# Performance work log

Measured on AMD Instinct MI355X. Metric: run time of the kernel, lower is better.

Reference implementation:

```python
import jax, jax.numpy as jnp
import numpy as np

N_OBJ = 256   # number of RoIs/objects
C = 151       # num_obj_classes (Visual Genome)
H = 512       # hidden_dim == output_dim
T = 3         # time_step


def setup_inputs() -> dict:
    key = jax.random.key(0)
    ks = jax.random.split(key, 12)
    s = jnp.float32(0.02)

    def lin(k, out_dim, in_dim):
        k1, k2 = jax.random.split(k)
        w = jax.random.normal(k1, (out_dim, in_dim), jnp.float32) * s
        b = jax.random.normal(k2, (out_dim,), jnp.float32) * s
        return w, b

    inp = {}
    inp['input_ggnn'] = jax.random.normal(ks[0], (N_OBJ, H), jnp.float32)
    inp['matrix'] = jax.random.uniform(ks[1], (C, C), jnp.float32)
    for i, name in enumerate(['eq3_w', 'eq3_u', 'eq4_w', 'eq4_u', 'eq5_w', 'eq5_u']):
        in_dim = 2 * H if name.endswith('_w') else H
        w, b = lin(ks[2 + i], H, in_dim)
        inp['w_' + name] = w
        inp['b_' + name] = b
    w, b = lin(ks[8], H, 2 * H)
    inp['w_out'], inp['b_out'] = w, b
    w, b = lin(ks[9], C, C * H)
    inp['w_cls'], inp['b_cls'] = w, b
    return inp


def _ggnn_obj(input_ggnn, matrix,
              w_eq3_w, b_eq3_w, w_eq3_u, b_eq3_u,
              w_eq4_w, b_eq4_w, w_eq4_u, b_eq4_u,
              w_eq5_w, b_eq5_w, w_eq5_u, b_eq5_u,
              w_out, b_out, w_cls, b_cls):
    n = input_ggnn.shape[0]
    # hidden[i, c] = input_ggnn[i] for every class slot c  -> [N, C, H]
    hidden0 = jnp.broadcast_to(input_ggnn[:, None, :], (n, C, H))

    def step(hidden, _):
        hidden_sum = hidden.sum(axis=0)                # [C, H]
        x = hidden_sum[None, :, :] - hidden            # [N, C, H]
        # matrix.T @ x_i  and  matrix @ x_i, vectorized over N
        av1 = jnp.einsum('cd,nch->ndh', matrix, x)     # M^T propagation
        av2 = jnp.einsum('dc,nch->ndh', matrix, x)     # M propagation
        av = jnp.concatenate([av1, av2], axis=-1).reshape(n * C, 2 * H)
        h = hidden.reshape(n * C, H)
        zv = jax.nn.sigmoid(av @ w_eq3_w.T + b_eq3_w + h @ w_eq3_u.T + b_eq3_u)
        rv = jax.nn.sigmoid(av @ w_eq4_w.T + b_eq4_w + h @ w_eq4_u.T + b_eq4_u)
        hv = jnp.tanh(av @ w_eq5_w.T + b_eq5_w + (rv * h) @ w_eq5_u.T + b_eq5_u)
        h = (1.0 - zv) * h + zv * hv
        return h.reshape(n, C, H), None

    hidden, _ = jax.lax.scan(step, hidden0, None, length=T)

    inp_rep = hidden0.reshape(n * C, H)                # input repeated per class slot
    out = jnp.concatenate([hidden.reshape(n * C, H), inp_rep], axis=1)  # [N*C, 2H]
    out = jax.nn.relu(out @ w_out.T + b_out)           # [N*C, H]
    obj_dists = out.reshape(n, C * H) @ w_cls.T + b_cls  # [N, C]
    return obj_dists


def reference(input_ggnn, matrix,
              w_eq3_w, b_eq3_w, w_eq3_u, b_eq3_u,
              w_eq4_w, b_eq4_w, w_eq4_u, b_eq4_u,
              w_eq5_w, b_eq5_w, w_eq5_u, b_eq5_u,
              w_out, b_out, w_cls, b_cls):
    return _ggnn_obj(input_ggnn, matrix,
                     w_eq3_w, b_eq3_w, w_eq3_u, b_eq3_u,
                     w_eq4_w, b_eq4_w, w_eq4_u, b_eq4_u,
                     w_eq5_w, b_eq5_w, w_eq5_u, b_eq5_u,
                     w_out, b_out, w_cls, b_cls)
```

## Files before the change

### kernel.cpp

```cpp
#include <hip/hip_runtime.h>


#define C_     151
#define H_     512
#define NOBJ   256
#define NR     38656
#define NCH    64
#define CH     9664
#define CHP    9728
#define KPAD   160
#define KLDS   168
#define KA     2560
#define KV     3584
#define KB     2560

typedef _Float16 half8 __attribute__((ext_vector_type(8)));
typedef _Float16 half4 __attribute__((ext_vector_type(4)));
typedef float    f32x4 __attribute__((ext_vector_type(4)));

__device__ __forceinline__ float sigm(float x) { return 1.f / (1.f + expf(-x)); }

__device__ __forceinline__ void gload16(const void* g, void* l) {
    __builtin_amdgcn_global_load_lds(
        (const __attribute__((address_space(1))) void*)g,
        (__attribute__((address_space(3))) void*)l, 16, 0, 0);
}

__device__ __forceinline__ int kqswz(int s) {
    return 8 * (((s & 3) + 8 - ((s >> 2) & 3) - ((s >> 4) & 3)) & 3);
}
__device__ __forceinline__ int fraswz(int lane) {
    const int lb = lane & 15;
    return lb * 32 + 8 * (((lane >> 4) + lb + (lb >> 2)) & 3);
}

__device__ __forceinline__ half8 loadA8(const _Float16* p) { return *(const half8*)p; }
__device__ __forceinline__ half8 loadA8(const float* p) {
    f32x4 a = *(const f32x4*)p;
    f32x4 b = *(const f32x4*)(p + 4);
    half8 o;
    #pragma unroll
    for (int j = 0; j < 4; ++j) { o[j] = (_Float16)a[j]; o[4 + j] = (_Float16)b[j]; }
    return o;
}

template<int OP, typename AT, bool DUPK>
__global__ __launch_bounds__(256, 2)
void gemm_kernel(const AT* __restrict__ A, int lda,
                 const _Float16* __restrict__ B, int ldb,
                 void* __restrict__ Out, int ldo,
                 const float* __restrict__ bias,
                 const float* __restrict__ bias2,
                 int kchunk, int chunkStride)
{
    constexpr bool A16 = (sizeof(AT) == 2);
    __shared__ _Float16 sA[128 * 32];
    __shared__ _Float16 sB[128 * 32];
    const int tid  = threadIdx.x;
    const int lane = tid & 63;
    const int w    = tid >> 6;
    const int m0   = blockIdx.x * 128;
    const int n0   = blockIdx.y * 128;
    const int kbase = blockIdx.z * kchunk;

    const int s0 = tid, s1 = tid + 256;
    const AT* Ap0 = A + (size_t)(m0 + (s0 >> 2)) * lda + kqswz(s0);
    const AT* Ap1 = A + (size_t)(m0 + (s1 >> 2)) * lda + kqswz(s1);
    const _Float16* Bp0 = B + (size_t)(n0 + (s0 >> 2)) * ldb + kbase + kqswz(s0);
    const _Float16* Bp1 = B + (size_t)(n0 + (s1 >> 2)) * ldb + kbase + kqswz(s1);
    const int la0 = 8 * s0;
    const int la1 = 8 * s1;
    _Float16* lA0 = &sA[w * 512];
    _Float16* lA1 = &sA[2048 + w * 512];
    _Float16* lB0 = &sB[w * 512];
    _Float16* lB1 = &sB[2048 + w * 512];

    f32x4 acc[4][4];
    #pragma unroll
    for (int i = 0; i < 4; ++i)
        #pragma unroll
        for (int j = 0; j < 4; ++j)
            #pragma unroll
            for (int r = 0; r < 4; ++r) acc[i][j][r] = 0.f;

    const int mrow = (w >> 1) * 64;
    const int ncol = (w & 1) * 64;
    const int fra  = fraswz(lane);

    for (int k0 = 0; k0 < kchunk; k0 += 32) {
        int kA;
        if (DUPK) kA = (k0 < 2048) ? k0 : ((k0 < 3072) ? k0 - 2048 : k0 - 1024);
        else      kA = kbase + k0;
        if constexpr (A16) {
            __syncthreads();
            gload16(Ap0 + kA, lA0);
            gload16(Ap1 + kA, lA1);
            gload16(Bp0 + k0, lB0);
            gload16(Bp1 + k0, lB1);
            __syncthreads();
        } else {
            half8 va0 = loadA8(Ap0 + kA);
            half8 va1 = loadA8(Ap1 + kA);
            half8 vb0 = *(const half8*)(Bp0 + k0);
            half8 vb1 = *(const half8*)(Bp1 + k0);
            __syncthreads();
            *(half8*)&sA[la0] = va0;
            *(half8*)&sA[la1] = va1;
            *(half8*)&sB[la0] = vb0;
            *(half8*)&sB[la1] = vb1;
            __syncthreads();
        }
        half8 af[4], bf[4];
        #pragma unroll
        for (int i = 0; i < 4; ++i)
            af[i] = *(const half8*)&sA[(mrow + i * 16) * 32 + fra];
        #pragma unroll
        for (int i = 0; i < 4; ++i)
            bf[i] = *(const half8*)&sB[(ncol + i * 16) * 32 + fra];
        #pragma unroll
        for (int mi = 0; mi < 4; ++mi)
            #pragma unroll
            for (int ni = 0; ni < 4; ++ni)
                acc[mi][ni] = __builtin_amdgcn_mfma_f32_16x16x32_f16(af[mi], bf[ni], acc[mi][ni], 0, 0, 0);
    }

    const size_t zoff = (size_t)blockIdx.z * (size_t)chunkStride;
    #pragma unroll
    for (int mi = 0; mi < 4; ++mi) {
        #pragma unroll
        for (int ni = 0; ni < 4; ++ni) {
            #pragma unroll
            for (int r = 0; r < 4; ++r) {
                const int row = m0 + mrow + mi * 16 + (lane >> 4) * 4 + r;
                const int col = n0 + ncol + ni * 16 + (lane & 15);
                float v = acc[mi][ni][r];
                const size_t o = zoff + (size_t)row * ldo + col;
                if (OP == 0) {
                    ((float*)Out)[o] = v;
                } else if (OP == 1) {
                    ((_Float16*)Out)[o] = (_Float16)v;
                } else {
                    const unsigned n = (unsigned)row / 151u;
                    v += bias[col] + bias2[n * 512u + col];
                    v = v > 0.f ? v : 0.f;
                    ((_Float16*)Out)[o] = (_Float16)v;
                }
            }
        }
    }
}

__global__ __launch_bounds__(512, 2)
void gemm256(const _Float16* __restrict__ A, const _Float16* __restrict__ B,
             _Float16* __restrict__ Out)
{
    constexpr int LDA = KA;
    constexpr int LDB = KB;
    constexpr int LDO = 1536;
    constexpr int NT  = KV / 64;
    __shared__ _Float16 lds[2][32768];

    const int tid  = threadIdx.x;
    const int lane = tid & 63;
    const int w    = tid >> 6;

    const int lin  = blockIdx.y * gridDim.x + blockIdx.x;
    const int xcd  = lin & 7;
    const int sub  = lin >> 3;
    const int wgid = (xcd < 4 ? xcd * 29 : 4 * 29 + (xcd - 4) * 28) + sub;
    const int m0   = (wgid / 6) * 256;
    const int n0   = (wgid % 6) * 256;

    const int tr  = tid >> 3;
    const int swz = ((tid & 7) ^ (tr & 7)) << 3;
    const _Float16* Ap = A + (size_t)(m0 + tr) * LDA + swz;
    const _Float16* Bp = B + (size_t)(n0 + tr) * LDB + swz;
    const int ldsbase = w << 9;

    auto stage = [&](int buf, int kAb, int kBb) {
        _Float16* L = &lds[buf][0];
        gload16(Ap + kAb,                        L + ldsbase);
        gload16(Ap + (size_t)128 * LDA + kAb,    L + 128 * 64 + ldsbase);
        gload16(Bp + kBb,                        L + 16384 + ldsbase);
        gload16(Bp + (size_t)64  * LDB + kBb,    L + 16384 +  64 * 64 + ldsbase);
        gload16(Bp + (size_t)128 * LDB + kBb,    L + 16384 + 128 * 64 + ldsbase);
        gload16(Bp + (size_t)192 * LDB + kBb,    L + 16384 + 192 * 64 + ldsbase);
        gload16(Ap + (size_t)64  * LDA + kAb,    L +  64 * 64 + ldsbase);
        gload16(Ap + (size_t)192 * LDA + kAb,    L + 192 * 64 + ldsbase);
    };

    const int lb = lane & 15;
    const int lq = lane >> 4;
    auto frag = [&](const _Float16* base, int row0, int ks) -> half8 {
        const int row = row0 + lb;
        const int kg  = ks * 4 + lq;
        return *(const half8*)&base[row * 64 + ((kg ^ (row & 7)) << 3)];
    };

    const int wm = (w >> 2) * 128;
    const int wn = (w & 3) * 64;

    f32x4 acc[8][4];
    #pragma unroll
    for (int i = 0; i < 8; ++i)
        #pragma unroll
        for (int j = 0; j < 4; ++j)
            #pragma unroll
            for (int r = 0; r < 4; ++r) acc[i][j][r] = 0.f;

    half8 aL[4][2], aH[4][2], bA[2][2], bB[2][2];

#define PHASE_MFMA(AF, BF, MO, NO) do {                                         \
    __builtin_amdgcn_s_setprio(1);                                              \
    _Pragma("unroll")                                                           \
    for (int i = 0; i < 4; ++i) {                                               \
        _Pragma("unroll")                                                       \
        for (int j = 0; j < 2; ++j) {                                           \
            _Pragma("unroll")                                                   \
            for (int ks = 0; ks < 2; ++ks)                                      \
                acc[(MO) + i][(NO) + j] =                                       \
                    __builtin_amdgcn_mfma_f32_16x16x32_f16(                     \
                        AF[i][ks], BF[j][ks], acc[(MO) + i][(NO) + j], 0, 0, 0);\
        }                                                                       \
    }                                                                           \
    __builtin_amdgcn_s_setprio(0);                                              \
} while (0)

    stage(0, 0, 0);

    for (int t = 0; t < NT; ++t) {
        const _Float16* sA = &lds[t & 1][0];
        const _Float16* sB = &lds[t & 1][16384];

        asm volatile("s_waitcnt vmcnt(2)" ::: "memory");
        __builtin_amdgcn_s_barrier();
        __builtin_amdgcn_sched_barrier(0);
        if (t + 1 < NT) {
            const int kk  = (t + 1) * 64;
            const int kAb = (kk < 2048) ? kk : ((kk < 3072) ? kk - 2048 : kk - 1024);
            const int kBb = (kk < 1024) ? kk : kk - 1024;
            stage((t + 1) & 1, kAb, kBb);
        }
        #pragma unroll
        for (int i = 0; i < 4; ++i) {
            aL[i][0] = frag(sA, wm + i * 16, 0);
            aL[i][1] = frag(sA, wm + i * 16, 1);
        }
        #pragma unroll
        for (int j = 0; j < 2; ++j) {
            bA[j][0] = frag(sB, wn + j * 16, 0);
            bA[j][1] = frag(sB, wn + j * 16, 1);
        }
        #pragma unroll
        for (int j = 0; j < 2; ++j) {
            bB[j][0] = frag(sB, wn + 32 + j * 16, 0);
            bB[j][1] = frag(sB, wn + 32 + j * 16, 1);
        }
        PHASE_MFMA(aL, bA, 0, 0);
        PHASE_MFMA(aL, bB, 0, 2);

        if (t + 1 < NT) asm volatile("s_waitcnt vmcnt(8)" ::: "memory");
        else            asm volatile("s_waitcnt vmcnt(0)" ::: "memory");
        __builtin_amdgcn_s_barrier();
        __builtin_amdgcn_sched_barrier(0);
        #pragma unroll
        for (int i = 0; i < 4; ++i) {
            aH[i][0] = frag(sA, wm + 64 + i * 16, 0);
            aH[i][1] = frag(sA, wm + 64 + i * 16, 1);
        }
        PHASE_MFMA(aH, bA, 4, 0);
        PHASE_MFMA(aH, bB, 4, 2);
    }
#undef PHASE_MFMA

    #pragma unroll
    for (int mi = 0; mi < 8; ++mi) {
        #pragma unroll
        for (int ni = 0; ni < 4; ++ni) {
            #pragma unroll
            for (int r = 0; r < 4; ++r) {
                const int row = m0 + wm + mi * 16 + (lane >> 4) * 4 + r;
                const int col = n0 + wn + ni * 16 + (lane & 15);
                Out[(size_t)row * LDO + col] = (_Float16)acc[mi][ni][r];
            }
        }
    }
}

__global__ __launch_bounds__(256, 2)
void mix_kernel(const float* __restrict__ hid, const float* __restrict__ S,
                const _Float16* __restrict__ MTh, const _Float16* __restrict__ MTl,
                const _Float16* __restrict__ Mrh, const _Float16* __restrict__ Mrl,
                _Float16* __restrict__ AVH, int cbase)
{
    __shared__ _Float16 sxh[64 * KLDS];
    __shared__ _Float16 sxl[64 * KLDS];
    const int n  = blockIdx.x;
    const int h0 = blockIdx.y * 64;
    const int tid = threadIdx.x;

    #pragma unroll
    for (int i = 0; i < 5; ++i) {
        const int s  = tid + 256 * i;
        const int c  = s >> 3;
        const int hg = s & 7;
        half8 oh, ol;
        if (c < C_) {
            const float* hp = &hid[(size_t)(cbase + n * C_ + c) * H_ + h0 + hg * 8];
            const float* sp = &S[c * H_ + h0 + hg * 8];
            half8 hh;
            #pragma unroll
            for (int j = 0; j < 8; ++j) {
                const float hv = hp[j];
                const float x = sp[j] - hv;
                const _Float16 hi = (_Float16)x;
                oh[j] = hi;
                ol[j] = (_Float16)(x - (float)hi);
                hh[j] = (_Float16)hv;
            }
            *(half8*)&AVH[(size_t)(n * C_ + c) * KA + 2048 + h0 + hg * 8] = hh;
        } else {
            #pragma unroll
            for (int j = 0; j < 8; ++j) { oh[j] = (_Float16)0.f; ol[j] = (_Float16)0.f; }
        }
        #pragma unroll
        for (int j = 0; j < 8; ++j) {
            sxh[(hg * 8 + j) * KLDS + c] = oh[j];
            sxl[(hg * 8 + j) * KLDS + c] = ol[j];
        }
    }
    __syncthreads();

    const int lane = tid & 63;
    const int w    = tid >> 6;
    const _Float16* Mhi = (w >> 1) ? Mrh : MTh;
    const _Float16* Mlo = (w >> 1) ? Mrl : MTl;
    const int hb = (w & 1) * 32;

    f32x4 acc[10][2];
    #pragma unroll
    for (int i = 0; i < 10; ++i)
        #pragma unroll
        for (int j = 0; j < 2; ++j)
            #pragma unroll
            for (int r = 0; r < 4; ++r) acc[i][j][r] = 0.f;

    #pragma unroll
    for (int pass = 0; pass < 3; ++pass) {
        const _Float16* Ma = (pass == 2) ? Mlo : Mhi;
        const _Float16* X  = (pass == 1) ? sxl : sxh;
        #pragma unroll
        for (int kk = 0; kk < 5; ++kk) {
            const int k0 = kk * 32;
            half8 bf[2];
            #pragma unroll
            for (int ht = 0; ht < 2; ++ht)
                bf[ht] = *(const half8*)&X[(hb + ht * 16 + (lane & 15)) * KLDS + k0 + 8 * (lane >> 4)];
            #pragma unroll
            for (int dt = 0; dt < 10; ++dt) {
                half8 af = *(const half8*)&Ma[(dt * 16 + (lane & 15)) * KPAD + k0 + 8 * (lane >> 4)];
                acc[dt][0] = __builtin_amdgcn_mfma_f32_16x16x32_f16(af, bf[0], acc[dt][0], 0, 0, 0);
                acc[dt][1] = __builtin_amdgcn_mfma_f32_16x16x32_f16(af, bf[1], acc[dt][1], 0, 0, 0);
            }
        }
    }

    const int mixoff = (w >> 1) * 512;
    #pragma unroll
    for (int dt = 0; dt < 10; ++dt) {
        #pragma unroll
        for (int ht = 0; ht < 2; ++ht) {
            #pragma unroll
            for (int r = 0; r < 4; ++r) {
                const int d = dt * 16 + (lane >> 4) * 4 + r;
                if (d < C_) {
                    const int h = h0 + hb + ht * 16 + (lane & 15);
                    const float v = acc[dt][ht][r];
                    const _Float16 hi = (_Float16)v;
                    const _Float16 lo = (_Float16)(v - (float)hi);
                    _Float16* rowp = AVH + (size_t)(n * C_ + d) * KA + mixoff + h;
                    rowp[0]    = hi;
                    rowp[1024] = lo;
                }
            }
        }
    }
}


__global__ void k_sreduce(const float* __restrict__ hid, float* __restrict__ Stmp)
{
    const int c  = blockIdx.x;
    const int g  = blockIdx.y;
    const int hw = threadIdx.x;
    const float* p = hid + (size_t)c * H_ + hw * 8;
    float s[8];
    #pragma unroll
    for (int j = 0; j < 8; ++j) s[j] = 0.f;
    const size_t stride = (size_t)C_ * H_;
    for (int n = g * 32; n < g * 32 + 32; ++n) {
        f32x4 a = *(const f32x4*)(p + (size_t)n * stride);
        f32x4 b = *(const f32x4*)(p + (size_t)n * stride + 4);
        #pragma unroll
        for (int j = 0; j < 4; ++j) { s[j] += a[j]; s[4 + j] += b[j]; }
    }
    float* o = Stmp + (size_t)g * (C_ * H_) + c * H_ + hw * 8;
    *(f32x4*)o       = f32x4{s[0], s[1], s[2], s[3]};
    *(f32x4*)(o + 4) = f32x4{s[4], s[5], s[6], s[7]};
}

__global__ void k_sfold(const float* __restrict__ Stmp, float* __restrict__ S)
{
    const int idx = blockIdx.x * 256 + threadIdx.x;
    float s = 0.f;
    #pragma unroll
    for (int g = 0; g < 8; ++g) s += Stmp[(size_t)g * (C_ * H_) + idx];
    S[idx] = s;
}

__global__ void k_ew1(_Float16* __restrict__ pre, const float* __restrict__ hid,
                      const float* __restrict__ bz, const float* __restrict__ br, int cbase)
{
    const int idx = blockIdx.x * 256 + threadIdx.x;
    const unsigned r = idx >> 7;
    const int o4 = (idx & 127) << 2;
    const size_t base = (size_t)r * 1536;
    half4 zp = *(const half4*)&pre[base + o4];
    half4 rp = *(const half4*)&pre[base + 512 + o4];
    f32x4 hd = *(const f32x4*)&hid[(size_t)(cbase + r) * H_ + o4];
    f32x4 bz4 = *(const f32x4*)&bz[o4];
    f32x4 br4 = *(const f32x4*)&br[o4];
    half4 zs, rh;
    #pragma unroll
    for (int j = 0; j < 4; ++j) {
        float z = sigm((float)zp[j] + bz4[j]);
        float rr = sigm((float)rp[j] + br4[j]);
        zs[j] = (_Float16)z;
        rh[j] = (_Float16)(rr * hd[j]);
    }
    *(half4*)&pre[base + o4] = zs;
    *(half4*)&pre[base + 512 + o4] = rh;
}

__global__ void k_ew2(const _Float16* __restrict__ pre, const _Float16* __restrict__ p5a,
                      const _Float16* __restrict__ p5b,
                      float* __restrict__ hid, const float* __restrict__ b5, int cbase)
{
    const int idx = blockIdx.x * 256 + threadIdx.x;
    const unsigned r = idx >> 7;
    const int o4 = (idx & 127) << 2;
    const size_t base = (size_t)r * 1536;
    half4 w5 = *(const half4*)&pre[base + 1024 + o4];
    half4 pa = *(const half4*)&p5a[(size_t)r * H_ + o4];
    half4 pb = *(const half4*)&p5b[(size_t)r * H_ + o4];
    half4 zz = *(const half4*)&pre[base + o4];
    f32x4 hd = *(const f32x4*)&hid[(size_t)(cbase + r) * H_ + o4];
    f32x4 b54 = *(const f32x4*)&b5[o4];
    #pragma unroll
    for (int j = 0; j < 4; ++j) {
        float t = tanhf((float)w5[j] + (float)pa[j] + (float)pb[j] + b54[j]);
        float z = (float)zz[j];
        hd[j] = (1.f - z) * hd[j] + z * t;
    }
    *(f32x4*)&hid[(size_t)(cbase + r) * H_ + o4] = hd;
}


__global__ void prep_wbig(const float* w3w, const float* w3u,
                          const float* w4w, const float* w4u,
                          const float* w5w, const float* w5u,
                          _Float16* __restrict__ Wbig)
{
    const int idx = blockIdx.x * 256 + threadIdx.x;
    const int op = idx / KB;
    const int j = idx - op * KB;
    const int g = op >> 9, o = op & 511;
    const float* ww = (g == 0) ? w3w : (g == 1) ? w4w : w5w;
    const float* wu = (g == 0) ? w3u : (g == 1) ? w4u : w5u;
    _Float16 out;
    if (j < 1024) {
        out = (_Float16)ww[o * 1024 + j];
    } else if (j < 2048) {
        const float v = ww[o * 1024 + (j - 1024)];
        const _Float16 hi = (_Float16)v;
        out = (_Float16)(v - (float)hi);
    } else {
        out = (g < 2) ? (_Float16)wu[o * 512 + (j - 2048)] : (_Float16)0.f;
    }
    Wbig[idx] = out;
}

__global__ void prep_m(const float* __restrict__ matrix,
                       _Float16* __restrict__ MTh, _Float16* __restrict__ MTl,
                       _Float16* __restrict__ Mrh, _Float16* __restrict__ Mrl)
{
    const int idx = blockIdx.x * 256 + threadIdx.x;
    const int d = idx / KPAD, c = idx - d * KPAD;
    float vT = 0.f, vR = 0.f;
    if (d < C_ && c < C_) { vT = matrix[c * C_ + d]; vR = matrix[d * C_ + c]; }
    const _Float16 th = (_Float16)vT;
    const _Float16 rh = (_Float16)vR;
    MTh[idx] = th; MTl[idx] = (_Float16)(vT - (float)th);
    Mrh[idx] = rh; Mrl[idx] = (_Float16)(vR - (float)rh);
}

__global__ void prep_wout(const float* __restrict__ wout,
                          _Float16* __restrict__ WL, _Float16* __restrict__ WR)
{
    const int idx = blockIdx.x * 256 + threadIdx.x;
    const int o = idx >> 9, j = idx & 511;
    WL[idx] = (_Float16)wout[o * 1024 + j];
    WR[idx] = (_Float16)wout[o * 1024 + 512 + j];
}

__global__ void prep_wcls(const float* __restrict__ wcls, _Float16* __restrict__ w16)
{
    const int k = blockIdx.x * 256 + threadIdx.x;
    const int d = blockIdx.y;
    w16[(size_t)d * (C_ * H_) + k] = (_Float16)wcls[(size_t)d * (C_ * H_) + k];
}

__global__ void k_cast(const float* __restrict__ src, _Float16* __restrict__ dst, int n)
{
    const int i = blockIdx.x * 256 + threadIdx.x;
    if (i < n) dst[i] = (_Float16)src[i];
}

__global__ void prep_bias(const float* b3w, const float* b3u, const float* b4w,
                          const float* b4u, const float* b5w, const float* b5u,
                          float* bz, float* br, float* b5)
{
    const int i = threadIdx.x;
    bz[i] = b3w[i] + b3u[i];
    br[i] = b4w[i] + b4u[i];
    b5[i] = b5w[i] + b5u[i];
}

__global__ void prep_hid(const float* __restrict__ input, float* __restrict__ hid)
{
    const int idx = blockIdx.x * 256 + threadIdx.x;
    const unsigned row = idx >> 7;
    const int h4 = (idx & 127) << 2;
    const unsigned n = row / 151u;
    f32x4 v = *(const f32x4*)&input[(size_t)n * H_ + h4];
    *(f32x4*)&hid[(size_t)row * H_ + h4] = v;
}

__global__ void k_reduce(const float* __restrict__ partial, const float* __restrict__ bcls,
                         float* __restrict__ out)
{
    const int idx = blockIdx.x * 256 + threadIdx.x;
    const unsigned n = (unsigned)idx / 151u;
    const unsigned d = (unsigned)idx - n * 151u;
    float s = 0.f;
    for (int z = 0; z < C_; ++z)
        s += partial[(size_t)z * (NOBJ * 256) + n * 256 + d];
    out[idx] = s + bcls[d];
}


extern "C" void kernel_launch(void* const* d_in, const int* in_sizes, int n_in,
                              void* d_out, int out_size, void* d_ws, size_t ws_size,
                              hipStream_t stream)
{
    const float* input  = (const float*)d_in[0];
    const float* matrix = (const float*)d_in[1];
    const float* w3w = (const float*)d_in[2];
    const float* b3w = (const float*)d_in[3];
    const float* w3u = (const float*)d_in[4];
    const float* b3u = (const float*)d_in[5];
    const float* w4w = (const float*)d_in[6];
    const float* b4w = (const float*)d_in[7];
    const float* w4u = (const float*)d_in[8];
    const float* b4u = (const float*)d_in[9];
    const float* w5w = (const float*)d_in[10];
    const float* b5w = (const float*)d_in[11];
    const float* w5u = (const float*)d_in[12];
    const float* b5u = (const float*)d_in[13];
    const float* wout = (const float*)d_in[14];
    const float* bout = (const float*)d_in[15];
    const float* wcls = (const float*)d_in[16];
    const float* bcls = (const float*)d_in[17];
    float* obj = (float*)d_out;

    char* ws = (char*)d_ws;
    size_t off = 0;
    auto take = [&](size_t bytes) -> char* {
        off = (off + 255) & ~(size_t)255;
        char* p = ws + off;
        off += bytes;
        return p;
    };

    _Float16* Wbig  = (_Float16*)take((size_t)1536 * KB * 2);
    _Float16* MTh   = (_Float16*)take((size_t)KPAD * KPAD * 2);
    _Float16* MTl   = (_Float16*)take((size_t)KPAD * KPAD * 2);
    _Float16* Mrh   = (_Float16*)take((size_t)KPAD * KPAD * 2);
    _Float16* Mrl   = (_Float16*)take((size_t)KPAD * KPAD * 2);
    _Float16* W5u16 = (_Float16*)take((size_t)512 * 512 * 2);
    _Float16* WL16  = (_Float16*)take((size_t)512 * 512 * 2);
    _Float16* WR16  = (_Float16*)take((size_t)512 * 512 * 2);
    _Float16* in16  = (_Float16*)take((size_t)256 * 512 * 2);
    float*    bz    = (float*)take(512 * 4);
    float*    br    = (float*)take(512 * 4);
    float*    b5    = (float*)take(512 * 4);
    float*    Stmp  = (float*)take((size_t)8 * C_ * H_ * 4);
    float*    S32   = (float*)take((size_t)C_ * H_ * 4);
    float*    base  = (float*)take((size_t)256 * 512 * 4);
    float*    hid32 = (float*)take((size_t)NR * H_ * 4);
    _Float16* AVH   = (_Float16*)take((size_t)CHP * KA * 2);
    _Float16* prec  = (_Float16*)take((size_t)CHP * 1536 * 2);
    _Float16* p5u = AVH;
    _Float16* OUT16 = AVH;
    _Float16* Wcls16 = (_Float16*)hid32;
    float* partial = (float*)((char*)hid32 + (size_t)NOBJ * C_ * H_ * 2);

    (void)in_sizes; (void)n_in; (void)out_size; (void)ws_size;

    prep_wbig<<<dim3((1536 * KB) / 256), 256, 0, stream>>>(w3w, w3u, w4w, w4u, w5w, w5u, Wbig);
    prep_m<<<dim3((KPAD * KPAD) / 256), 256, 0, stream>>>(matrix, MTh, MTl, Mrh, Mrl);
    k_cast<<<dim3((512 * 512) / 256), 256, 0, stream>>>(w5u, W5u16, 512 * 512);
    prep_wout<<<dim3((512 * 512) / 256), 256, 0, stream>>>(wout, WL16, WR16);
    k_cast<<<dim3((256 * 512) / 256), 256, 0, stream>>>(input, in16, 256 * 512);
    prep_bias<<<dim3(1), 512, 0, stream>>>(b3w, b3u, b4w, b4u, b5w, b5u, bz, br, b5);
    prep_hid<<<dim3((NR * 128) / 256), 256, 0, stream>>>(input, hid32);
    gemm_kernel<0, _Float16, false><<<dim3(2, 4, 1), 256, 0, stream>>>(
        in16, 512, WR16, 512, base, 512, nullptr, nullptr, 512, 0);

    for (int t = 0; t < 3; ++t) {
        k_sreduce<<<dim3(C_, 8), 64, 0, stream>>>(hid32, Stmp);
        k_sfold<<<dim3((C_ * H_) / 256), 256, 0, stream>>>(Stmp, S32);
        for (int cc = 0; cc < 4; ++cc) {
            const int cbase = cc * CH;
            mix_kernel<<<dim3(NCH, 8), 256, 0, stream>>>(
                hid32, S32, MTh, MTl, Mrh, Mrl, AVH, cbase);
            gemm256<<<dim3(CHP / 256, 1536 / 256, 1), 512, 0, stream>>>(
                AVH, Wbig, prec);
            k_ew1<<<dim3((CH * 128) / 256), 256, 0, stream>>>(prec, hid32, bz, br, cbase);
            gemm_kernel<1, _Float16, false><<<dim3(CHP / 128, 4, 2), 256, 0, stream>>>(
                prec + 512, 1536, W5u16, 512, p5u, 512, nullptr, nullptr, 256, CHP * 512);
            k_ew2<<<dim3((CH * 128) / 256), 256, 0, stream>>>(
                prec, p5u, p5u + (size_t)CHP * 512, hid32, b5, cbase);
        }
    }

    gemm_kernel<2, float, false><<<dim3(NR / 128, 512 / 128, 1), 256, 0, stream>>>(
        hid32, 512, WL16, 512, OUT16, 512, bout, base, 512, 0);

    prep_wcls<<<dim3((C_ * H_) / 256, C_), 256, 0, stream>>>(wcls, Wcls16);
    gemm_kernel<0, _Float16, false><<<dim3(NOBJ / 128, 256 / 128, C_), 256, 0, stream>>>(
        OUT16, C_ * H_, Wcls16, C_ * H_, partial, 256, nullptr, nullptr, 512, NOBJ * 256);
    k_reduce<<<dim3(NR / 256), 256, 0, stream>>>(partial, bcls, obj);
}
```

Before: 2.416 ms.

## Load GEMM B fragments directly into registers, keep only A in LDS

The gemm256 kernel now stages only the A tile through LDS. Each wave loads its B fragments straight from global memory into double-buffered registers, prefetching the next K-tile while computing the current one. This halves the LDS footprint, which may let two workgroups fit per CU. It also removes the mid-tile barrier and wait. In exchange it adds register pressure on top of the already large accumulator set, and waves sharing columns issue duplicate global B reads that rely on cache hits.

```diff
diff --git a/kernel.cpp b/kernel.cpp
--- a/kernel.cpp
+++ b/kernel.cpp
@@ -158,7 +158,7 @@
     constexpr int LDB = KB;
     constexpr int LDO = 1536;
     constexpr int NT  = KV / 64;
-    __shared__ _Float16 lds[2][32768];
+    __shared__ _Float16 lds[2][16384];
 
     const int tid  = threadIdx.x;
     const int lane = tid & 63;
@@ -174,19 +174,14 @@
     const int tr  = tid >> 3;
     const int swz = ((tid & 7) ^ (tr & 7)) << 3;
     const _Float16* Ap = A + (size_t)(m0 + tr) * LDA + swz;
-    const _Float16* Bp = B + (size_t)(n0 + tr) * LDB + swz;
     const int ldsbase = w << 9;
 
-    auto stage = [&](int buf, int kAb, int kBb) {
+    auto stageA = [&](int buf, int kAb) {
         _Float16* L = &lds[buf][0];
-        gload16(Ap + kAb,                        L + ldsbase);
-        gload16(Ap + (size_t)128 * LDA + kAb,    L + 128 * 64 + ldsbase);
-        gload16(Bp + kBb,                        L + 16384 + ldsbase);
-        gload16(Bp + (size_t)64  * LDB + kBb,    L + 16384 +  64 * 64 + ldsbase);
-        gload16(Bp + (size_t)128 * LDB + kBb,    L + 16384 + 128 * 64 + ldsbase);
-        gload16(Bp + (size_t)192 * LDB + kBb,    L + 16384 + 192 * 64 + ldsbase);
-        gload16(Ap + (size_t)64  * LDA + kAb,    L +  64 * 64 + ldsbase);
-        gload16(Ap + (size_t)192 * LDA + kAb,    L + 192 * 64 + ldsbase);
+        gload16(Ap + kAb,                     L + ldsbase);
+        gload16(Ap + (size_t)64  * LDA + kAb, L +  64 * 64 + ldsbase);
+        gload16(Ap + (size_t)128 * LDA + kAb, L + 128 * 64 + ldsbase);
+        gload16(Ap + (size_t)192 * LDA + kAb, L + 192 * 64 + ldsbase);
     };
 
     const int lb = lane & 15;
@@ -200,6 +195,8 @@
     const int wm = (w >> 2) * 128;
     const int wn = (w & 3) * 64;
 
+    const _Float16* Bb = B + (size_t)(n0 + wn + lb) * LDB + lq * 8;
+
     f32x4 acc[8][4];
     #pragma unroll
     for (int i = 0; i < 8; ++i)
@@ -208,7 +205,20 @@
             #pragma unroll
             for (int r = 0; r < 4; ++r) acc[i][j][r] = 0.f;
 
-    half8 aL[4][2], aH[4][2], bA[2][2], bB[2][2];
+    half8 a[4][2];
+    half8 b0A[2][2], b0B[2][2];
+    half8 b1A[2][2], b1B[2][2];
+
+#define LOADB(BA, BBb, kBb) do {                                                \
+    _Pragma("unroll")                                                           \
+    for (int j = 0; j < 2; ++j) {                                               \
+        _Pragma("unroll")                                                       \
+        for (int ks = 0; ks < 2; ++ks) {                                        \
+            BA[j][ks]  = *(const half8*)(Bb + (size_t)(j * 16) * LDB + (kBb) + ks * 32);       \
+            BBb[j][ks] = *(const half8*)(Bb + (size_t)(32 + j * 16) * LDB + (kBb) + ks * 32);  \
+        }                                                                       \
+    }                                                                           \
+} while (0)
 
 #define PHASE_MFMA(AF, BF, MO, NO) do {                                         \
     __builtin_amdgcn_s_setprio(1);                                              \
@@ -226,51 +236,47 @@
     __builtin_amdgcn_s_setprio(0);                                              \
 } while (0)
 
-    stage(0, 0, 0);
-
-    for (int t = 0; t < NT; ++t) {
-        const _Float16* sA = &lds[t & 1][0];
-        const _Float16* sB = &lds[t & 1][16384];
-
-        asm volatile("s_waitcnt vmcnt(2)" ::: "memory");
-        __builtin_amdgcn_s_barrier();
-        __builtin_amdgcn_sched_barrier(0);
-        if (t + 1 < NT) {
-            const int kk  = (t + 1) * 64;
-            const int kAb = (kk < 2048) ? kk : ((kk < 3072) ? kk - 2048 : kk - 1024);
-            const int kBb = (kk < 1024) ? kk : kk - 1024;
-            stage((t + 1) & 1, kAb, kBb);
-        }
-        #pragma unroll
-        for (int i = 0; i < 4; ++i) {
-            aL[i][0] = frag(sA, wm + i * 16, 0);
-            aL[i][1] = frag(sA, wm + i * 16, 1);
-        }
-        #pragma unroll
-        for (int j = 0; j < 2; ++j) {
-            bA[j][0] = frag(sB, wn + j * 16, 0);
-            bA[j][1] = frag(sB, wn + j * 16, 1);
-        }
-        #pragma unroll
-        for (int j = 0; j < 2; ++j) {
-            bB[j][0] = frag(sB, wn + 32 + j * 16, 0);
-            bB[j][1] = frag(sB, wn + 32 + j * 16, 1);
-        }
-        PHASE_MFMA(aL, bA, 0, 0);
-        PHASE_MFMA(aL, bB, 0, 2);
-
-        if (t + 1 < NT) asm volatile("s_waitcnt vmcnt(8)" ::: "memory");
-        else            asm volatile("s_waitcnt vmcnt(0)" ::: "memory");
-        __builtin_amdgcn_s_barrier();
-        __builtin_amdgcn_sched_barrier(0);
-        #pragma unroll
-        for (int i = 0; i < 4; ++i) {
-            aH[i][0] = frag(sA, wm + 64 + i * 16, 0);
-            aH[i][1] = frag(sA, wm + 64 + i * 16, 1);
-        }
-        PHASE_MFMA(aH, bA, 4, 0);
-        PHASE_MFMA(aH, bB, 4, 2);
-    }
+#define TILE(T, PF, CURBUF, NXTBUF, BCA, BCB, BNA, BNB) do {                    \
+    asm volatile("s_waitcnt vmcnt(8)" ::: "memory");                            \
+    __builtin_amdgcn_s_barrier();                                               \
+    __builtin_amdgcn_sched_barrier(0);                                          \
+    if (PF) {                                                                   \
+        const int kk  = ((T) + 1) * 64;                                         \
+        const int kAb = (kk < 2048) ? kk : ((kk < 3072) ? kk - 2048 : kk - 1024);\
+        const int kBb = (kk < 1024) ? kk : kk - 1024;                           \
+        stageA(NXTBUF, kAb);                                                    \
+        LOADB(BNA, BNB, kBb);                                                   \
+    }                                                                           \
+    {                                                                           \
+        const _Float16* sA_ = &lds[CURBUF][0];                                  \
+        _Pragma("unroll")                                                       \
+        for (int i = 0; i < 4; ++i) {                                           \
+            a[i][0] = frag(sA_, wm + i * 16, 0);                                \
+            a[i][1] = frag(sA_, wm + i * 16, 1);                                \
+        }                                                                       \
+        PHASE_MFMA(a, BCA, 0, 0);                                               \
+        PHASE_MFMA(a, BCB, 0, 2);                                               \
+        _Pragma("unroll")                                                       \
+        for (int i = 0; i < 4; ++i) {                                           \
+            a[i][0] = frag(sA_, wm + 64 + i * 16, 0);                           \
+            a[i][1] = frag(sA_, wm + 64 + i * 16, 1);                           \
+        }                                                                       \
+        PHASE_MFMA(a, BCA, 4, 0);                                               \
+        PHASE_MFMA(a, BCB, 4, 2);                                               \
+    }                                                                           \
+} while (0)
+
+    stageA(0, 0);
+    LOADB(b0A, b0B, 0);
+
+    for (int t2 = 0; t2 + 2 < NT; t2 += 2) {
+        TILE(t2,     1, 0, 1, b0A, b0B, b1A, b1B);
+        TILE(t2 + 1, 1, 1, 0, b1A, b1B, b0A, b0B);
+    }
+    TILE(NT - 2, 1, 0, 1, b0A, b0B, b1A, b1B);
+    TILE(NT - 1, 0, 1, 0, b1A, b1B, b0A, b0B);
+#undef TILE
+#undef LOADB
 #undef PHASE_MFMA
 
     #pragma unroll
```

After: 3.082 ms. 27.6% more time.

## Interleave next-tile global-to-LDS loads across four MFMA phases in GEMM loop

Applied to the files above, without the earlier changes.

Splits the per-iteration staging of the next K tile into four pairs of global_load_lds issues, interleaved between the four MFMA phases with extra barriers and lgkmcnt waits. The A fragment registers are reused for the low and high halves, which reduces register pressure. The goal is to spread memory issue across the compute phases, similar to an 8-wave ping-pong schedule. The cost is more barriers per iteration. The vmcnt accounting is delicate because the waits now depend on the load order, so a mistake could stall the loop or read LDS before the data has landed.

```diff
diff --git a/kernel.cpp b/kernel.cpp
--- a/kernel.cpp
+++ b/kernel.cpp
@@ -177,16 +177,11 @@
     const _Float16* Bp = B + (size_t)(n0 + tr) * LDB + swz;
     const int ldsbase = w << 9;
 
-    auto stage = [&](int buf, int kAb, int kBb) {
-        _Float16* L = &lds[buf][0];
-        gload16(Ap + kAb,                        L + ldsbase);
-        gload16(Ap + (size_t)128 * LDA + kAb,    L + 128 * 64 + ldsbase);
-        gload16(Bp + kBb,                        L + 16384 + ldsbase);
-        gload16(Bp + (size_t)64  * LDB + kBb,    L + 16384 +  64 * 64 + ldsbase);
-        gload16(Bp + (size_t)128 * LDB + kBb,    L + 16384 + 128 * 64 + ldsbase);
-        gload16(Bp + (size_t)192 * LDB + kBb,    L + 16384 + 192 * 64 + ldsbase);
-        gload16(Ap + (size_t)64  * LDA + kAb,    L +  64 * 64 + ldsbase);
-        gload16(Ap + (size_t)192 * LDA + kAb,    L + 192 * 64 + ldsbase);
+    auto stA = [&](int buf, int kAb, int r0) {
+        gload16(Ap + (size_t)r0 * LDA + kAb, &lds[buf][r0 * 64 + ldsbase]);
+    };
+    auto stB = [&](int buf, int kBb, int r0) {
+        gload16(Bp + (size_t)r0 * LDB + kBb, &lds[buf][16384 + r0 * 64 + ldsbase]);
     };
 
     const int lb = lane & 15;
@@ -208,7 +203,7 @@
             #pragma unroll
             for (int r = 0; r < 4; ++r) acc[i][j][r] = 0.f;
 
-    half8 aL[4][2], aH[4][2], bA[2][2], bB[2][2];
+    half8 a[4][2], bA[2][2], bB[2][2];
 
 #define PHASE_MFMA(AF, BF, MO, NO) do {                                         \
     __builtin_amdgcn_s_setprio(1);                                              \
@@ -226,50 +221,71 @@
     __builtin_amdgcn_s_setprio(0);                                              \
 } while (0)
 
-    stage(0, 0, 0);
+    stB(0, 0, 0);  stB(0, 0, 64);  stB(0, 0, 128); stB(0, 0, 192);
+    stA(0, 0, 0);  stA(0, 0, 128); stA(0, 0, 64);  stA(0, 0, 192);
+    asm volatile("s_waitcnt vmcnt(2)" ::: "memory");
+    __builtin_amdgcn_s_barrier();
+    __builtin_amdgcn_sched_barrier(0);
 
     for (int t = 0; t < NT; ++t) {
         const _Float16* sA = &lds[t & 1][0];
         const _Float16* sB = &lds[t & 1][16384];
-
-        asm volatile("s_waitcnt vmcnt(2)" ::: "memory");
-        __builtin_amdgcn_s_barrier();
-        __builtin_amdgcn_sched_barrier(0);
-        if (t + 1 < NT) {
-            const int kk  = (t + 1) * 64;
-            const int kAb = (kk < 2048) ? kk : ((kk < 3072) ? kk - 2048 : kk - 1024);
-            const int kBb = (kk < 1024) ? kk : kk - 1024;
-            stage((t + 1) & 1, kAb, kBb);
-        }
+        const int nb = (t + 1) & 1;
+        const bool pf = (t + 1 < NT);
+        int kAb = 0, kBb = 0;
+        if (pf) {
+            const int kk = (t + 1) * 64;
+            kAb = (kk < 2048) ? kk : ((kk < 3072) ? kk - 2048 : kk - 1024);
+            kBb = (kk < 1024) ? kk : kk - 1024;
+        }
+
         #pragma unroll
         for (int i = 0; i < 4; ++i) {
-            aL[i][0] = frag(sA, wm + i * 16, 0);
-            aL[i][1] = frag(sA, wm + i * 16, 1);
+            a[i][0] = frag(sA, wm + i * 16, 0);
+            a[i][1] = frag(sA, wm + i * 16, 1);
         }
         #pragma unroll
         for (int j = 0; j < 2; ++j) {
             bA[j][0] = frag(sB, wn + j * 16, 0);
             bA[j][1] = frag(sB, wn + j * 16, 1);
         }
+        if (pf) { stB(nb, kBb, 0); stB(nb, kBb, 64); }
+        __builtin_amdgcn_s_barrier();
+        asm volatile("s_waitcnt lgkmcnt(0)" ::: "memory");
+        PHASE_MFMA(a, bA, 0, 0);
+        __builtin_amdgcn_s_barrier();
+
         #pragma unroll
         for (int j = 0; j < 2; ++j) {
             bB[j][0] = frag(sB, wn + 32 + j * 16, 0);
             bB[j][1] = frag(sB, wn + 32 + j * 16, 1);
         }
-        PHASE_MFMA(aL, bA, 0, 0);
-        PHASE_MFMA(aL, bB, 0, 2);
-
-        if (t + 1 < NT) asm volatile("s_waitcnt vmcnt(8)" ::: "memory");
-        else            asm volatile("s_waitcnt vmcnt(0)" ::: "memory");
+        if (pf) { stB(nb, kBb, 128); stB(nb, kBb, 192); }
+        __builtin_amdgcn_s_barrier();
+        asm volatile("s_waitcnt lgkmcnt(0)" ::: "memory");
+        PHASE_MFMA(a, bB, 0, 2);
+        if (pf) asm volatile("s_waitcnt vmcnt(4)" ::: "memory");
+        else    asm volatile("s_waitcnt vmcnt(0)" ::: "memory");
         __builtin_amdgcn_s_barrier();
         __builtin_amdgcn_sched_barrier(0);
+
         #pragma unroll
         for (int i = 0; i < 4; ++i) {
-            aH[i][0] = frag(sA, wm + 64 + i * 16, 0);
-            aH[i][1] = frag(sA, wm + 64 + i * 16, 1);
-        }
-        PHASE_MFMA(aH, bA, 4, 0);
-        PHASE_MFMA(aH, bB, 4, 2);
+            a[i][0] = frag(sA, wm + 64 + i * 16, 0);
+            a[i][1] = frag(sA, wm + 64 + i * 16, 1);
+        }
+        if (pf) { stA(nb, kAb, 0); stA(nb, kAb, 128); }
+        __builtin_amdgcn_s_barrier();
+        asm volatile("s_waitcnt lgkmcnt(0)" ::: "memory");
+        PHASE_MFMA(a, bA, 4, 0);
+        __builtin_amdgcn_s_barrier();
+
+        if (pf) { stA(nb, kAb, 64); stA(nb, kAb, 192); }
+        __builtin_amdgcn_s_barrier();
+        PHASE_MFMA(a, bB, 4, 2);
+        asm volatile("s_waitcnt vmcnt(2)" ::: "memory");
+        __builtin_amdgcn_s_barrier();
+        __builtin_amdgcn_sched_barrier(0);
     }
 #undef PHASE_MFMA
 
```

New measurement: 2.440 ms. No clear change (+1.0%).
